# Kernel optimization log

Hardware: AMD Instinct MI355X
Metric: run time of the kernel (lower is better)

The kernel has to match this reference:

```python
import jax, jax.numpy as jnp
import numpy as np

D_MODEL = 1024
B, N = 8, 2048

def setup_inputs() -> dict:
    key = jax.random.key(0)
    k1, k2, k3 = jax.random.split(key, 3)
    x = jax.random.normal(k1, (B, N, D_MODEL), dtype=jnp.float32)
    W_qkv = jax.random.normal(k2, (3 * D_MODEL, D_MODEL), dtype=jnp.float32) * (D_MODEL ** -0.5)
    b_qkv = jax.random.normal(k3, (3 * D_MODEL,), dtype=jnp.float32) * 0.02
    return {"x": x, "W_qkv": W_qkv, "b_qkv": b_qkv}

def reference(x, W_qkv, b_qkv):
    d = x.shape[-1]
    scale = d ** 0.5
    # qkv projection: torch Linear computes x @ W.T + b
    qkv = jnp.einsum('bnc,oc->bno', x, W_qkv) + b_qkv  # [B, N, 3d]
    q, k, v = jnp.split(qkv, 3, axis=-1)               # each [B, N, d]
    scores = jnp.einsum('bqd,bkd->bqk', q, k) / scale  # [B, N, N]
    attn = jax.nn.softmax(scores, axis=-1)
    return jnp.einsum('bqk,bkd->bqd', attn, v)         # [B, N, d]
```

## Files before the change

kernel.cpp:

```cpp
#include <hip/hip_runtime.h>


#define AS1 __attribute__((address_space(1)))
#define AS3 __attribute__((address_space(3)))

typedef __bf16 bfrag  __attribute__((ext_vector_type(8)));
typedef float  ffrag  __attribute__((ext_vector_type(4)));
typedef __bf16 bf16x4 __attribute__((ext_vector_type(4)));

__global__ __launch_bounds__(256) void cvt_fused(const float* __restrict__ x,
                                                 const float* __restrict__ W,
                                                 __bf16* __restrict__ xb,
                                                 __bf16* __restrict__ Wb,
                                                 float* __restrict__ rowsum) {
  const int gid = blockIdx.x * 256 + threadIdx.x;
  const int stride = gridDim.x * 256;
  for (int k = gid; k < 4194304; k += stride) {
    float4 v = ((const float4*)x)[k];
    bf16x4 o;
    o[0] = (__bf16)v.x; o[1] = (__bf16)v.y; o[2] = (__bf16)v.z; o[3] = (__bf16)v.w;
    ((bf16x4*)xb)[k] = o;
  }
  for (int k = gid; k < 786432; k += stride) {
    float4 v = ((const float4*)W)[k];
    bf16x4 o;
    o[0] = (__bf16)v.x; o[1] = (__bf16)v.y; o[2] = (__bf16)v.z; o[3] = (__bf16)v.w;
    ((bf16x4*)Wb)[k] = o;
  }
  for (int k = gid; k < 16384; k += stride) rowsum[k] = 0.0f;
}

__device__ __forceinline__ void stage_half(
    const __bf16* __restrict__ Atile, const __bf16* __restrict__ Btile,
    int lda, int ldb, __bf16* lds, int tid, int te, int h) {
  const int kt = te * 64;
  const __bf16* src = (h < 2) ? Atile : Btile;
  const int ld = (h < 2) ? lda : ldb;
  const int row0 = (h & 1) * 128;
  __bf16* dst = lds + (te & 1) * 32768 + h * 8192;
#pragma unroll
  for (int l = 0; l < 2; ++l) {
    const int y = l * 4096 + tid * 8;
    const int r = y >> 6;
    const int c = ((tid & 7) * 8) ^ ((r & 7) << 3);
    __builtin_amdgcn_global_load_lds((AS1 void*)(src + (size_t)(row0 + r) * ld + kt + c),
                                     (AS3 void*)(dst + y), 16, 0, 0);
  }
}

template <int QA>
__device__ __forceinline__ void rd_a(const __bf16* lds, int bufoff, int aRowBase,
                                     int ck0, int ck1, bfrag a[4][2]) {
#pragma unroll
  for (int m = 0; m < 4; ++m) {
    const int off = bufoff + aRowBase + QA * 8192 + m * 1024;
    a[m][0] = *(const bfrag*)&lds[off + ck0];
    a[m][1] = *(const bfrag*)&lds[off + ck1];
  }
}

template <int QB>
__device__ __forceinline__ void rd_bq(const __bf16* lds, int bufoff, int bRowBase,
                                      int ck0, int ck1, bfrag b[2][2]) {
#pragma unroll
  for (int n = 0; n < 2; ++n) {
    const int off = bufoff + bRowBase + QB * 8192 + n * 1024;
    b[n][0] = *(const bfrag*)&lds[off + ck0];
    b[n][1] = *(const bfrag*)&lds[off + ck1];
  }
}

#define PH(QA, QB, BREG, DOVM)                                                 \
  {                                                                            \
    if (DOVM) asm volatile("s_waitcnt vmcnt(6)" ::: "memory");                 \
    __builtin_amdgcn_s_barrier();                                              \
    asm volatile("s_waitcnt lgkmcnt(0)" ::: "memory");                         \
    __builtin_amdgcn_s_setprio(1);                                             \
    _Pragma("unroll") for (int m_ = 0; m_ < 4; ++m_)                           \
    _Pragma("unroll") for (int n_ = 0; n_ < 2; ++n_)                           \
    _Pragma("unroll") for (int ks_ = 0; ks_ < 2; ++ks_)                        \
      acc[(QA) * 4 + m_][(QB) * 2 + n_] =                                      \
          __builtin_amdgcn_mfma_f32_16x16x32_bf16(                             \
              a[m_][ks_], BREG[n_][ks_], acc[(QA) * 4 + m_][(QB) * 2 + n_],    \
              0, 0, 0);                                                        \
    __builtin_amdgcn_s_setprio(0);                                             \
  }

#define STG(TE, H) stage_half(Atile, Btile, lda, ldb, lds, tid, (TE), (H))

__device__ __forceinline__ void gemm256_mainloop(
    const __bf16* __restrict__ Atile, const __bf16* __restrict__ Btile,
    int lda, int ldb, int K, __bf16* lds, ffrag acc[8][4]) {
  const int tid  = threadIdx.x;
  const int lane = tid & 63;
  const int wid  = tid >> 6;
  const int wr   = wid >> 2, wc = wid & 3;
  const int fr   = lane & 15;
  const int fk   = (lane >> 4) * 8;
  const int swz  = (fr & 7) << 3;
  const int ck0  = fk ^ swz;
  const int ck1  = (32 + fk) ^ swz;
  const int aRowBase = (wr * 64 + fr) * 64;
  const int bRowBase = 16384 + (wc * 32 + fr) * 64;
  const int nT = K >> 6;

  STG(0, 0); STG(0, 2); STG(0, 3); STG(0, 1);
  STG(1, 0); STG(1, 2); STG(1, 3);
  asm volatile("s_waitcnt vmcnt(6)" ::: "memory");
  __builtin_amdgcn_s_barrier();

  const int nIter = nT >> 1;
#pragma unroll 1
  for (int i = 0; i < nIter; ++i) {
    const int t1  = 2 * i + 1;
    const int t2e = (2 * i + 2 < nT) ? (2 * i + 2) : (2 * i);
    const int t3e = (2 * i + 3 < nT) ? (2 * i + 3) : (2 * i + 1);
    bfrag a[4][2], b0f[2][2], b1f[2][2];
    rd_a<0>(lds, 0, aRowBase, ck0, ck1, a);
    rd_bq<0>(lds, 0, bRowBase, ck0, ck1, b0f);
    STG(t1, 1);
    PH(0, 0, b0f, false)
    rd_bq<1>(lds, 0, bRowBase, ck0, ck1, b1f);
    PH(0, 1, b1f, false)
    rd_a<1>(lds, 0, aRowBase, ck0, ck1, a);
    STG(t2e, 0);
    PH(1, 1, b1f, false)
    STG(t2e, 2);
    STG(t2e, 3);
    PH(1, 0, b0f, true)
    rd_a<0>(lds, 32768, aRowBase, ck0, ck1, a);
    rd_bq<0>(lds, 32768, bRowBase, ck0, ck1, b0f);
    STG(t2e, 1);
    PH(0, 0, b0f, false)
    rd_bq<1>(lds, 32768, bRowBase, ck0, ck1, b1f);
    PH(0, 1, b1f, false)
    rd_a<1>(lds, 32768, aRowBase, ck0, ck1, a);
    STG(t3e, 0);
    STG(t3e, 2);
    PH(1, 1, b1f, false)
    STG(t3e, 3);
    PH(1, 0, b0f, true)
  }
}

#define ACC_ZERO()                                                             \
  ffrag acc[8][4];                                                             \
  _Pragma("unroll") for (int m = 0; m < 8; ++m)                                \
  _Pragma("unroll") for (int n = 0; n < 4; ++n) acc[m][n] = (ffrag)(0.0f);


__global__ __launch_bounds__(512, 1) void qkv_gemm256(
    const __bf16* __restrict__ Abf, const __bf16* __restrict__ Wbf,
    const float* __restrict__ bias,
    __bf16* __restrict__ Q, __bf16* __restrict__ Ko, __bf16* __restrict__ Vt) {
  __shared__ __bf16 lds[65536];
  ACC_ZERO();
  int bid = (int)blockIdx.x;
  bid = (bid & 7) * 96 + (bid >> 3);
  const int brow = (bid / 12) * 256;
  const int bcol = (bid % 12) * 256;
  gemm256_mainloop(Abf + (size_t)brow * 1024, Wbf + (size_t)bcol * 1024,
                   1024, 1024, 1024, lds, acc);
  const int lane = threadIdx.x & 63, wid = threadIdx.x >> 6;
  const int wr = wid >> 2, wc = wid & 3;
  const int region = bcol >> 10;
  if (region < 2) {
    __bf16* dst = region == 0 ? Q : Ko;
    const float scale = region == 0 ? 0.03125f : 1.0f;
#pragma unroll
    for (int j = 0; j < 4; ++j) {
      const int qb = j >> 1, n = j & 1;
      const int col = bcol + qb * 128 + wc * 32 + n * 16 + (lane & 15);
      const int o = col & 1023;
      const float bv = bias[col];
#pragma unroll
      for (int i = 0; i < 8; ++i) {
        const int qa = i >> 2, m = i & 3;
#pragma unroll
        for (int r = 0; r < 4; ++r) {
          const int mg = brow + qa * 128 + wr * 64 + m * 16 + (lane >> 4) * 4 + r;
          dst[(size_t)mg * 1024 + o] = (__bf16)((acc[i][j][r] + bv) * scale);
        }
      }
    }
  } else {
#pragma unroll
    for (int j = 0; j < 4; ++j) {
      const int qb = j >> 1, n = j & 1;
      const int col = bcol + qb * 128 + wc * 32 + n * 16 + (lane & 15);
      const int o = col & 1023;
      const float bv = bias[col];
#pragma unroll
      for (int i = 0; i < 8; ++i) {
        const int qa = i >> 2, m = i & 3;
        const int mg0 = brow + qa * 128 + wr * 64 + m * 16 + (lane >> 4) * 4;
        const int b = mg0 >> 11, nr = mg0 & 2047;
        bf16x4 v;
#pragma unroll
        for (int r = 0; r < 4; ++r) v[r] = (__bf16)(acc[i][j][r] + bv);
        *(bf16x4*)&Vt[(size_t)b * 2097152 + (size_t)o * 2048 + nr] = v;
      }
    }
  }
}

__global__ __launch_bounds__(512, 1) void scores_gemm256(const __bf16* __restrict__ Q,
                                                         const __bf16* __restrict__ Kb,
                                                         __bf16* __restrict__ Pu,
                                                         float* __restrict__ rowsum) {
  __shared__ __bf16 lds[65536];
  ACC_ZERO();
  int bid = (int)blockIdx.x;
  const int wg = (bid & 7) * 64 + (bid >> 3);
  const int brow = (wg & 7) * 256, bcol = ((wg >> 3) & 7) * 256, z = wg >> 6;
  gemm256_mainloop(Q + (size_t)z * 2048 * 1024 + (size_t)brow * 1024,
                   Kb + (size_t)z * 2048 * 1024 + (size_t)bcol * 1024,
                   1024, 1024, 1024, lds, acc);
  const int lane = threadIdx.x & 63, wid = threadIdx.x >> 6;
  const int wr = wid >> 2, wc = wid & 3;
  const int fr = lane & 15, g4 = (lane >> 4) * 4;
#pragma unroll
  for (int i = 0; i < 8; ++i) {
    const int qa = i >> 2, m = i & 3;
#pragma unroll
    for (int r = 0; r < 4; ++r) {
      const int mg = brow + qa * 128 + wr * 64 + m * 16 + g4 + r;
      float part = 0.0f;
#pragma unroll
      for (int j = 0; j < 4; ++j) {
        const int qb = j >> 1, n = j & 1;
        const int o = bcol + qb * 128 + wc * 32 + n * 16 + fr;
        const float e = __expf(acc[i][j][r] - 16.0f);
        part += e;
        Pu[((size_t)(z * 2048 + mg)) * 2048 + o] = (__bf16)e;
      }
      part += __shfl_xor(part, 1, 64);
      part += __shfl_xor(part, 2, 64);
      part += __shfl_xor(part, 4, 64);
      part += __shfl_xor(part, 8, 64);
      if (fr == 0) atomicAdd(&rowsum[z * 2048 + mg], part);
    }
  }
}

__global__ __launch_bounds__(512, 1) void pv_gemm256(const __bf16* __restrict__ P,
                                                     const __bf16* __restrict__ Vt,
                                                     const float* __restrict__ rowsum,
                                                     float* __restrict__ O) {
  __shared__ __bf16 lds[65536];
  ACC_ZERO();
  int bid = (int)blockIdx.x;
  const int wg = (bid & 7) * 32 + (bid >> 3);
  const int brow = (wg & 7) * 256, bcol = ((wg >> 3) & 3) * 256, z = wg >> 5;
  gemm256_mainloop(P + (size_t)(z * 2048 + brow) * 2048,
                   Vt + (size_t)z * 1024 * 2048 + (size_t)bcol * 2048,
                   2048, 2048, 2048, lds, acc);
  const int lane = threadIdx.x & 63, wid = threadIdx.x >> 6;
  const int wr = wid >> 2, wc = wid & 3;
  const int fr = lane & 15, g4 = (lane >> 4) * 4;
#pragma unroll
  for (int i = 0; i < 8; ++i) {
    const int qa = i >> 2, m = i & 3;
#pragma unroll
    for (int r = 0; r < 4; ++r) {
      const int mg = brow + qa * 128 + wr * 64 + m * 16 + g4 + r;
      const float inv = 1.0f / rowsum[z * 2048 + mg];
#pragma unroll
      for (int j = 0; j < 4; ++j) {
        const int qb = j >> 1, n = j & 1;
        const int o = bcol + qb * 128 + wc * 32 + n * 16 + fr;
        O[((size_t)(z * 2048 + mg)) * 1024 + o] = acc[i][j][r] * inv;
      }
    }
  }
}

extern "C" void kernel_launch(void* const* d_in, const int* in_sizes, int n_in,
                              void* d_out, int out_size, void* d_ws, size_t ws_size,
                              hipStream_t stream) {
  (void)in_sizes; (void)n_in; (void)out_size; (void)ws_size;
  const float* x    = (const float*)d_in[0];
  const float* W    = (const float*)d_in[1];
  const float* bias = (const float*)d_in[2];
  float* out = (float*)d_out;
  char* ws = (char*)d_ws;
  const size_t MB = 1u << 20;
  __bf16* x_bf = (__bf16*)(ws + 0);
  __bf16* W_bf = (__bf16*)(ws + 32 * MB);
  __bf16* Qb   = (__bf16*)(ws + 38 * MB);
  __bf16* Kb   = (__bf16*)(ws + 70 * MB);
  __bf16* Pu   = (__bf16*)(ws + 102 * MB);
  __bf16* Vt   = (__bf16*)(ws + 166 * MB);
  float* rowsum = (float*)(ws + 198 * MB);

  cvt_fused<<<2048, 256, 0, stream>>>(x, W, x_bf, W_bf, rowsum);
  qkv_gemm256<<<768, 512, 0, stream>>>(x_bf, W_bf, bias, Qb, Kb, Vt);
  scores_gemm256<<<512, 512, 0, stream>>>(Qb, Kb, Pu, rowsum);
  pv_gemm256<<<256, 512, 0, stream>>>(Pu, Vt, rowsum, out);
}
```

Measured before the change: 245.9 us.

## Restructure GEMM mainloop into two-phase schedule with one-tile prefetch depth

Rewrites the 256x256 GEMM mainloop so each half-tile phase runs 16 MFMAs over both B quarters, instead of four 8-MFMA phases per tile. The prefetch depth drops from roughly 1.5 tiles to one tile ahead, and the vmcnt waits are retuned (6/2) to match. The aim is fewer barriers and waitcnt stalls per K-step, in exchange for less latency hiding on global loads and higher register pressure from holding b0f and b1f at once.

```diff
diff --git a/kernel.cpp b/kernel.cpp
--- a/kernel.cpp
+++ b/kernel.cpp
@@ -70,19 +70,20 @@
   }
 }
 
-#define PH(QA, QB, BREG, DOVM)                                                 \
+#define PH2(QA, VMC)                                                           \
   {                                                                            \
-    if (DOVM) asm volatile("s_waitcnt vmcnt(6)" ::: "memory");                 \
+    asm volatile("s_waitcnt vmcnt(" #VMC ")" ::: "memory");                    \
     __builtin_amdgcn_s_barrier();                                              \
     asm volatile("s_waitcnt lgkmcnt(0)" ::: "memory");                         \
     __builtin_amdgcn_s_setprio(1);                                             \
     _Pragma("unroll") for (int m_ = 0; m_ < 4; ++m_)                           \
     _Pragma("unroll") for (int n_ = 0; n_ < 2; ++n_)                           \
-    _Pragma("unroll") for (int ks_ = 0; ks_ < 2; ++ks_)                        \
-      acc[(QA) * 4 + m_][(QB) * 2 + n_] =                                      \
-          __builtin_amdgcn_mfma_f32_16x16x32_bf16(                             \
-              a[m_][ks_], BREG[n_][ks_], acc[(QA) * 4 + m_][(QB) * 2 + n_],    \
-              0, 0, 0);                                                        \
+    _Pragma("unroll") for (int ks_ = 0; ks_ < 2; ++ks_) {                      \
+      acc[(QA) * 4 + m_][n_] = __builtin_amdgcn_mfma_f32_16x16x32_bf16(        \
+          a[m_][ks_], b0f[n_][ks_], acc[(QA) * 4 + m_][n_], 0, 0, 0);          \
+      acc[(QA) * 4 + m_][2 + n_] = __builtin_amdgcn_mfma_f32_16x16x32_bf16(    \
+          a[m_][ks_], b1f[n_][ks_], acc[(QA) * 4 + m_][2 + n_], 0, 0, 0);      \
+    }                                                                          \
     __builtin_amdgcn_s_setprio(0);                                             \
   }
 
@@ -105,8 +106,7 @@
   const int nT = K >> 6;
 
   STG(0, 0); STG(0, 2); STG(0, 3); STG(0, 1);
-  STG(1, 0); STG(1, 2); STG(1, 3);
-  asm volatile("s_waitcnt vmcnt(6)" ::: "memory");
+  asm volatile("s_waitcnt vmcnt(2)" ::: "memory");
   __builtin_amdgcn_s_barrier();
 
   const int nIter = nT >> 1;
@@ -114,32 +114,23 @@
   for (int i = 0; i < nIter; ++i) {
     const int t1  = 2 * i + 1;
     const int t2e = (2 * i + 2 < nT) ? (2 * i + 2) : (2 * i);
-    const int t3e = (2 * i + 3 < nT) ? (2 * i + 3) : (2 * i + 1);
     bfrag a[4][2], b0f[2][2], b1f[2][2];
     rd_a<0>(lds, 0, aRowBase, ck0, ck1, a);
     rd_bq<0>(lds, 0, bRowBase, ck0, ck1, b0f);
+    rd_bq<1>(lds, 0, bRowBase, ck0, ck1, b1f);
+    STG(t1, 0); STG(t1, 2); STG(t1, 3);
+    PH2(0, 6)
+    rd_a<1>(lds, 0, aRowBase, ck0, ck1, a);
     STG(t1, 1);
-    PH(0, 0, b0f, false)
-    rd_bq<1>(lds, 0, bRowBase, ck0, ck1, b1f);
-    PH(0, 1, b1f, false)
-    rd_a<1>(lds, 0, aRowBase, ck0, ck1, a);
-    STG(t2e, 0);
-    PH(1, 1, b1f, false)
-    STG(t2e, 2);
-    STG(t2e, 3);
-    PH(1, 0, b0f, true)
+    PH2(1, 2)
     rd_a<0>(lds, 32768, aRowBase, ck0, ck1, a);
     rd_bq<0>(lds, 32768, bRowBase, ck0, ck1, b0f);
+    rd_bq<1>(lds, 32768, bRowBase, ck0, ck1, b1f);
+    STG(t2e, 0); STG(t2e, 2); STG(t2e, 3);
+    PH2(0, 6)
+    rd_a<1>(lds, 32768, aRowBase, ck0, ck1, a);
     STG(t2e, 1);
-    PH(0, 0, b0f, false)
-    rd_bq<1>(lds, 32768, bRowBase, ck0, ck1, b1f);
-    PH(0, 1, b1f, false)
-    rd_a<1>(lds, 32768, aRowBase, ck0, ck1, a);
-    STG(t3e, 0);
-    STG(t3e, 2);
-    PH(1, 1, b1f, false)
-    STG(t3e, 3);
-    PH(1, 0, b0f, true)
+    PH2(1, 2)
   }
 }
 
```

Result: no change. 246.2 us (+0.1%).
